# Optimization experiments

Hardware: AMD Instinct MI355X
Metric: run time of the kernel (lower is better)

The kernel has to match this reference:

```python
import jax, jax.numpy as jnp
import numpy as np

DN = ('NCHW', 'OIHW', 'NCHW')
EPS = 1e-5


def _conv(x, w, b, stride, pad):
    y = jax.lax.conv_general_dilated(x, w, (stride, stride), ((pad, pad), (pad, pad)), dimension_numbers=DN)
    return y + b[None, :, None, None]


def _convT(x, w, b):
    # PyTorch ConvTranspose2d(k=3, stride=2, padding=1, output_padding=1)
    # weight w: [in, out, kh, kw] -> flip spatial, swap in/out -> OIHW
    wt = jnp.flip(w, (2, 3)).transpose(1, 0, 2, 3)
    y = jax.lax.conv_general_dilated(x, wt, (1, 1), ((1, 2), (1, 2)), lhs_dilation=(2, 2), dimension_numbers=DN)
    return y + b[None, :, None, None]


def _inorm(x):
    # InstanceNorm2d, affine=False, biased variance (num_features arg unused since no affine)
    m = x.mean((2, 3), keepdims=True)
    v = ((x - m) ** 2).mean((2, 3), keepdims=True)
    return (x - m) / jnp.sqrt(v + EPS)


def _lrelu(x):
    return jnp.where(x >= 0, x, 0.2 * x)


def _refpad(x):
    return jnp.pad(x, ((0, 0), (0, 0), (1, 1), (1, 1)), mode='reflect')


def _backbone(image, w1, b1, w2, b2, w3, b3, wt, bt, w4, b4):
    x = _lrelu(_inorm(_conv(_refpad(image), w1, b1, 1, 0)))   # [B,32,H,W]
    x = _lrelu(_inorm(_conv(x, w2, b2, 2, 1)))                 # [B,64,H/2,W/2]
    x = _lrelu(_inorm(_conv(x, w3, b3, 2, 1)))                 # [B,128,H/4,W/4]
    x = _lrelu(_inorm(_convT(x, wt, bt)))                      # [B,256,H/2,W/2]
    x = jnp.tanh(_conv(_refpad(x), w4, b4, 1, 0))              # [B,512,H/2,W/2]
    return x


def _style_codes(x, seg):
    # nearest interpolation of seg to (h,w): src_idx = floor(dst * H / h)
    B, C, h, w = x.shape
    H, W = seg.shape[2], seg.shape[3]
    rows = (np.arange(h) * H) // h
    cols = (np.arange(w) * W) // w
    seg_ds = seg[:, :, rows][:, :, :, cols]                    # [B,L,h,w]
    m = (seg_ds != 0).astype(x.dtype)
    sums = jnp.einsum('bchw,blhw->blc', x, m)                  # segment sums
    counts = m.sum((2, 3))[..., None]                          # [B,L,1]
    return jnp.where(counts > 0, sums / jnp.maximum(counts, 1.0), 0.0)


def setup_inputs():
    key = jax.random.key(0)
    ks = jax.random.split(key, 8)
    B, H, W, L = 8, 256, 256, 19
    image = jax.random.normal(ks[0], (B, 3, H, W), jnp.float32)
    labels = jax.random.randint(ks[1], (B, H, W), 0, L)
    seg = jax.nn.one_hot(labels, L, axis=1, dtype=jnp.float32)  # one-hot semantic map
    def w(k, shape):
        return jax.random.normal(k, shape, jnp.float32) * 0.05
    return {
        'image': image, 'seg': seg,
        'w1': w(ks[2], (32, 3, 3, 3)), 'b1': jnp.zeros(32, jnp.float32),
        'w2': w(ks[3], (64, 32, 3, 3)), 'b2': jnp.zeros(64, jnp.float32),
        'w3': w(ks[4], (128, 64, 3, 3)), 'b3': jnp.zeros(128, jnp.float32),
        'wt': w(ks[5], (128, 256, 3, 3)), 'bt': jnp.zeros(256, jnp.float32),
        'w4': w(ks[6], (512, 256, 3, 3)), 'b4': jnp.zeros(512, jnp.float32),
    }


def reference(image, seg, w1, b1, w2, b2, w3, b3, wt, bt, w4, b4):
    x = _backbone(image, w1, b1, w2, b2, w3, b3, wt, bt, w4, b4)
    return _style_codes(x, seg)  # [B, label_nc, 512]
```

## Files before the change

### kernel.cpp

```cpp
#include <hip/hip_runtime.h>
#include <hip/hip_bf16.h>
#include <math.h>

typedef __attribute__((ext_vector_type(8))) short bf16x8;
typedef __attribute__((ext_vector_type(8))) unsigned short u16x8;
typedef __attribute__((ext_vector_type(4))) float f32x4;
typedef __attribute__((ext_vector_type(2))) long longx2;

#define OFF_X1   0ull
#define OFF_XQ8  0ull
#define OFF_X2   34080768ull
#define OFF_X3   51386368ull
#define OFF_Y4   60039168ull
#define OFF_WB8  127148032ull
#define OFF_WB2  129507328ull
#define OFF_WB3  129548288ull
#define OFF_WBT  129695744ull
#define OFF_ST1  130744320ull
#define OFF_ST2  130746368ull
#define OFF_ST3  130750464ull
#define OFF_ST4  130758656ull
#define OFF_SUMS 130775040ull
#define OFF_CNT  131086336ull
#define OFF_MS1  131086944ull
#define OFF_MS2  131088992ull
#define OFF_MS3  131093088ull
#define OFF_MS4  131101280ull
#define OFF_LAB  131117664ull
#define OFF_DWS  131641952ull
#define OFF_WSM  132166240ull
#define OFF_ST5  132690528ull
#define OFF_CB   132706912ull

__device__ __forceinline__ float bfu2f(unsigned short u) {
  return __builtin_bit_cast(float, ((unsigned)u) << 16);
}
__device__ __forceinline__ unsigned short f2bfu(float f) {
  __hip_bfloat16 h = __float2bfloat16(f);
  return __builtin_bit_cast(unsigned short, h);
}
__device__ __forceinline__ void gload_lds16(const void* g, void* l) {
  __builtin_amdgcn_global_load_lds(
      (const __attribute__((address_space(1))) unsigned int*)g,
      (__attribute__((address_space(3))) unsigned int*)l, 16, 0, 0);
}
template <bool HI>
__device__ __forceinline__ int cvtpk8(float a, float b, int old) {
  return __builtin_amdgcn_cvt_pk_fp8_f32(a, b, old, HI);
}
template <int SEL>
__device__ __forceinline__ float cvtf8(int v) {
  return __builtin_amdgcn_cvt_f32_fp8(v, SEL);
}

#define WAITV(N) asm volatile("s_waitcnt vmcnt(" #N ")" ::: "memory")

#define PIPE_STEP(WAITN, BUF, DOSTAGE, SNEXT)                 \
  asm volatile("s_waitcnt vmcnt(" #WAITN ")" ::: "memory");   \
  __builtin_amdgcn_s_barrier();                               \
  __builtin_amdgcn_sched_barrier(0);                          \
  mmaStep(BUF, (BUF) + 16384);                                \
  __builtin_amdgcn_sched_barrier(0);                          \
  __builtin_amdgcn_s_barrier();                               \
  if (DOSTAGE) stage(SNEXT, BUF);

__global__ __launch_bounds__(256) void padz_k(unsigned short* __restrict__ x1,
                                              unsigned short* __restrict__ x2,
                                              unsigned short* __restrict__ x3) {
  int u = blockIdx.x * 256 + threadIdx.x;
  int b = u / 10368, r = u % 10368;
  u16x8 z = {0, 0, 0, 0, 0, 0, 0, 0};
  if (r < 4128) {
    unsigned short* base = x1 + (size_t)b * 2130048;
    if (r < 2064) {
      int row = r < 1032 ? 0 : 257, pos = r < 1032 ? r : r - 1032;
      base += (row * 258 + (pos >> 2)) * 32 + (pos & 3) * 8;
    } else {
      int rc = r - 2064;
      int col = rc < 1032 ? 0 : 257, pos = rc < 1032 ? rc : rc - 1032;
      base += ((pos >> 2) * 258 + col) * 32 + (pos & 3) * 8;
    }
    *(u16x8*)base = z;
  } else if (r < 8288) {
    int s = r - 4128;
    unsigned short* base = x2 + (size_t)b * 1081600;
    if (s < 2080) {
      int row = s < 1040 ? 0 : 129, pos = s < 1040 ? s : s - 1040;
      base += (row * 130 + (pos >> 3)) * 64 + (pos & 7) * 8;
    } else {
      int sc = s - 2080;
      int col = sc < 1040 ? 0 : 129, pos = sc < 1040 ? sc : sc - 1040;
      base += ((pos >> 3) * 130 + col) * 64 + (pos & 7) * 8;
    }
    *(u16x8*)base = z;
  } else {
    int t = r - 8288;
    unsigned short* base = x3 + (size_t)b * 540800;
    if (t < 1040) {
      base += (64 * 65 + (t >> 4)) * 128 + (t & 15) * 8;
    } else {
      int pos = t - 1040;
      base += ((pos >> 4) * 65 + 64) * 128 + (pos & 15) * 8;
    }
    *(u16x8*)base = z;
  }
}

__global__ __launch_bounds__(256) void conv1_k(const float* __restrict__ img,
                                               const float* __restrict__ w1,
                                               unsigned short* __restrict__ x1) {
  __shared__ float wl[864];
  int t = threadIdx.x, y = blockIdx.x, b = blockIdx.y;
  for (int i = t; i < 864; i += 256) wl[i] = w1[(i & 31) * 27 + (i >> 5)];
  __syncthreads();
  int x = t;
  float val[27];
  for (int ic = 0; ic < 3; ++ic) {
    const float* ip = img + ((size_t)(b * 3 + ic)) * 65536;
#pragma unroll
    for (int ky = 0; ky < 3; ++ky) {
      int gy = y - 1 + ky; gy = gy < 0 ? -gy : (gy > 255 ? 510 - gy : gy);
#pragma unroll
      for (int kx = 0; kx < 3; ++kx) {
        int gx = x - 1 + kx; gx = gx < 0 ? -gx : (gx > 255 ? 510 - gx : gx);
        val[ic * 9 + ky * 3 + kx] = ip[gy * 256 + gx];
      }
    }
  }
  float a[32];
#pragma unroll
  for (int oc = 0; oc < 32; ++oc) a[oc] = 0.f;
#pragma unroll
  for (int k = 0; k < 27; ++k) {
    float vv = val[k];
#pragma unroll
    for (int oc = 0; oc < 32; ++oc) a[oc] += wl[k * 32 + oc] * vv;
  }
  unsigned short ov[32];
#pragma unroll
  for (int oc = 0; oc < 32; ++oc) ov[oc] = f2bfu(a[oc]);
  unsigned short* op = x1 + ((size_t)(b * 258 + y + 1) * 258 + (x + 1)) * 32;
#pragma unroll
  for (int i = 0; i < 4; ++i) *(u16x8*)(op + i * 8) = *(const u16x8*)(ov + i * 8);
}

template <int C>
__global__ void statsn_k(const unsigned short* __restrict__ base, int rowStride, int unitsLog,
                         int rowsPer, long bStride, float* __restrict__ stats) {
  const int CH8 = C / 8;
  __shared__ float bins[C * 2];
  int tid = threadIdx.x, slice = blockIdx.x, b = blockIdx.y;
  for (int i = tid; i < C * 2; i += 256) bins[i] = 0.f;
  __syncthreads();
  const unsigned short* bp = base + (size_t)b * bStride + (size_t)(slice * rowsPer) * rowStride;
  int total = rowsPer << unitsLog;
  float s8[8] = {0, 0, 0, 0, 0, 0, 0, 0}, q8[8] = {0, 0, 0, 0, 0, 0, 0, 0};
  for (int idx = tid; idx < total; idx += 256) {
    int rl = idx >> unitsLog, ux = idx & ((1 << unitsLog) - 1);
    u16x8 v = *(const u16x8*)(bp + (size_t)rl * rowStride + ux * 8);
#pragma unroll
    for (int e = 0; e < 8; ++e) { float f = bfu2f(v[e]); s8[e] += f; q8[e] += f * f; }
  }
#pragma unroll
  for (int e = 0; e < 8; ++e)
    for (int off = 32; off >= CH8; off >>= 1) {
      s8[e] += __shfl_xor(s8[e], off);
      q8[e] += __shfl_xor(q8[e], off);
    }
  int lane = tid & 63;
  if (lane < CH8) {
#pragma unroll
    for (int e = 0; e < 8; ++e) {
      atomicAdd(&bins[(lane * 8 + e) * 2], s8[e]);
      atomicAdd(&bins[(lane * 8 + e) * 2 + 1], q8[e]);
    }
  }
  __syncthreads();
  for (int i = tid; i < C * 2; i += 256) atomicAdd(&stats[b * C * 2 + i], bins[i]);
}

__global__ void msn_k(const float* __restrict__ st, float2* __restrict__ ms, float invN, int total) {
  int i = blockIdx.x * 256 + threadIdx.x;
  if (i < total) {
    float m = st[2 * i] * invN;
    float v = st[2 * i + 1] * invN - m * m;
    ms[i] = make_float2(m, rsqrtf(fmaxf(v, 0.f) + 1e-5f));
  }
}

template <int C>
__global__ void nln_k(unsigned short* __restrict__ base, int rowStride, int unitsPerRow,
                      long bStride, const float2* __restrict__ ms) {
  const int CH8 = C / 8;
  int row = blockIdx.x, b = blockIdx.y;
  unsigned short* rp = base + (size_t)b * bStride + (size_t)row * rowStride;
  const float2* msb = ms + b * C;
  for (int idx = threadIdx.x; idx < unitsPerRow; idx += 256) {
    u16x8 v = *(u16x8*)(rp + idx * 8);
    int ch = (idx & (CH8 - 1)) * 8;
    u16x8 o;
#pragma unroll
    for (int e = 0; e < 8; ++e) {
      float2 m = msb[ch + e];
      float f = (bfu2f(v[e]) - m.x) * m.y;
      o[e] = f2bfu(f >= 0.f ? f : 0.2f * f);
    }
    *(u16x8*)(rp + idx * 8) = o;
  }
}

__global__ __launch_bounds__(256) void nln8_k(const unsigned short* __restrict__ y4,
                                              const float2* __restrict__ ms,
                                              unsigned char* __restrict__ xq8,
                                              float* __restrict__ st5) {
  __shared__ float bs[512];
  int t = threadIdx.x, row = blockIdx.x, b = blockIdx.y;
  int cg = t & 31, pg = t >> 5;
  int wof0 = (cg >> 4) * 128 + ((((cg & 15) & 3) << 2) | ((cg & 15) >> 2)) * 8;
  const float2* msb = ms + b * 256;
  float2 m0[8];
#pragma unroll
  for (int e = 0; e < 8; ++e) m0[e] = msb[cg * 8 + e];
  const unsigned short* rp = y4 + ((size_t)b * 16384 + row * 128) * 256;
  unsigned char* op = xq8 + ((size_t)b * 16384 + (size_t)row * 128) * 256;
  float s[8] = {0, 0, 0, 0, 0, 0, 0, 0}, d[8] = {0, 0, 0, 0, 0, 0, 0, 0};
  for (int i = 0; i < 16; ++i) {
    int px = pg * 16 + i;
    u16x8 v = *(const u16x8*)(rp + (size_t)px * 256 + cg * 8);
    float f[8];
#pragma unroll
    for (int e = 0; e < 8; ++e) {
      float x = (bfu2f(v[e]) - m0[e].x) * m0[e].y;
      f[e] = x >= 0.f ? x : 0.2f * x;
    }
    int lo = cvtpk8<false>(f[0], f[1], 0); lo = cvtpk8<true>(f[2], f[3], lo);
    int hi = cvtpk8<false>(f[4], f[5], 0); hi = cvtpk8<true>(f[6], f[7], hi);
    *(long*)(op + (size_t)px * 256 + wof0) =
        ((long)(unsigned)hi << 32) | (unsigned)lo;
    float fq;
    fq = cvtf8<0>(lo); s[0] += fq; d[0] += fq - f[0];
    fq = cvtf8<1>(lo); s[1] += fq; d[1] += fq - f[1];
    fq = cvtf8<2>(lo); s[2] += fq; d[2] += fq - f[2];
    fq = cvtf8<3>(lo); s[3] += fq; d[3] += fq - f[3];
    fq = cvtf8<0>(hi); s[4] += fq; d[4] += fq - f[4];
    fq = cvtf8<1>(hi); s[5] += fq; d[5] += fq - f[5];
    fq = cvtf8<2>(hi); s[6] += fq; d[6] += fq - f[6];
    fq = cvtf8<3>(hi); s[7] += fq; d[7] += fq - f[7];
  }
  for (int i = t; i < 512; i += 256) bs[i] = 0.f;
  __syncthreads();
#pragma unroll
  for (int e = 0; e < 8; ++e) {
    atomicAdd(&bs[cg * 8 + e], s[e]);
    atomicAdd(&bs[256 + cg * 8 + e], d[e]);
  }
  __syncthreads();
  for (int i = t; i < 512; i += 256) atomicAdd(&st5[b * 512 + i], bs[i]);
}

__global__ void wrep2_k(const float* __restrict__ w2, unsigned short* __restrict__ wb2) {
  int idx = blockIdx.x * 256 + threadIdx.x;
  if (idx >= 20480) return;
  int oc = idx / 320, r = idx % 320, tap = r >> 5, ic = r & 31;
  wb2[idx] = tap < 9 ? f2bfu(w2[(oc * 32 + ic) * 9 + tap]) : (unsigned short)0;
}
__global__ void wrep3_k(const float* __restrict__ w3, unsigned short* __restrict__ wb3) {
  int idx = blockIdx.x * 256 + threadIdx.x;
  int oc = idx / 576, r = idx % 576, tap = r >> 6, ic = r & 63;
  wb3[idx] = f2bfu(w3[(oc * 64 + ic) * 9 + tap]);
}
__device__ const int c_taptab[16] = {4, -1, -1, -1, 5, 3, -1, -1, 7, -1, 1, -1, 8, 6, 2, 0};
__global__ void wrepT_k(const float* __restrict__ wt, unsigned short* __restrict__ wbt) {
  int idx = blockIdx.x * 256 + threadIdx.x;
  int n = idx >> 9, k = idx & 511;
  int cl = n >> 8, oc = n & 255, nb = k >> 7, ic = k & 127;
  int tap = c_taptab[cl * 4 + nb];
  wbt[idx] = tap < 0 ? (unsigned short)0 : f2bfu(wt[(ic * 256 + oc) * 9 + tap]);
}
__global__ __launch_bounds__(256) void dwrep_k(const float* __restrict__ w4,
                                               unsigned char* __restrict__ wb8,
                                               float* __restrict__ dws,
                                               float* __restrict__ wsum) {
  int oc = blockIdx.x, ic = threadIdx.x;
  int local = ic & 127;
  int p = (ic & 128) + ((local >> 3) & 3) * 32 + ((local >> 5) & 3) * 8 + (local & 7);
  float ds = 0.f, ws = 0.f;
  for (int kk = 0; kk < 9; ++kk) {
    float w = w4[(size_t)oc * 2304 + ic * 9 + kk];
    int pk = cvtpk8<false>(w, 0.f, 0);
    wb8[((size_t)oc * 9 + kk) * 256 + p] = (unsigned char)(pk & 0xff);
    float wq = cvtf8<0>(pk);
    ds += wq - w; ws += w;
  }
  dws[oc * 256 + ic] = ds;
  wsum[oc * 256 + ic] = ws;
}

__global__ __launch_bounds__(256) void cbias_k(const float* __restrict__ st5,
                                               const float* __restrict__ dws,
                                               const float* __restrict__ wsum,
                                               float* __restrict__ cb) {
  int oc = blockIdx.x, b = blockIdx.y, t = threadIdx.x;
  const float inv = 1.f / 16384.f;
  float muq = st5[b * 512 + t] * inv;
  float dmu = st5[b * 512 + 256 + t] * inv;
  float a = muq * dws[oc * 256 + t] + dmu * wsum[oc * 256 + t];
#pragma unroll
  for (int o = 1; o < 64; o <<= 1) a += __shfl_xor(a, o);
  __shared__ float r[4];
  if ((t & 63) == 0) r[t >> 6] = a;
  __syncthreads();
  if (t == 0) cb[b * 512 + oc] = r[0] + r[1] + r[2] + r[3];
}

__global__ __launch_bounds__(256) void conv2_k(const unsigned short* __restrict__ x1,
                                               const unsigned short* __restrict__ wb2,
                                               unsigned short* __restrict__ x2,
                                               float* __restrict__ st2) {
  __shared__ char smem[49664];
  float* bins = (float*)(smem + 49152);
  int tid = threadIdx.x, y = blockIdx.x, b = blockIdx.y;
  int lane = tid & 63, w = tid >> 6, wm = w >> 1, wn = w & 1;
  int lr = lane & 15, lg = lane >> 4;
  f32x4 acc[4][2];
#pragma unroll
  for (int i = 0; i < 4; ++i)
#pragma unroll
    for (int j = 0; j < 2; ++j) acc[i][j] = (f32x4){0.f, 0.f, 0.f, 0.f};

  int rowA[4], lcA[4], PbA[4];
#pragma unroll
  for (int i = 0; i < 4; ++i) {
    int pb = i * 256 + tid;
    PbA[i] = pb * 16; rowA[i] = pb >> 3; lcA[i] = (pb & 7) ^ (rowA[i] & 7);
  }
  int rowB[2], lcB[2], PbB[2];
#pragma unroll
  for (int i = 0; i < 2; ++i) {
    int pb = i * 256 + tid;
    PbB[i] = pb * 16; rowB[i] = pb >> 3; lcB[i] = (pb & 7) ^ (rowB[i] & 7);
  }
  const unsigned short* xb = x1 + (size_t)b * 2130048;

  auto stage = [&](int kb, char* base) {
    char* As = base;
    char* Bs = base + 16384;
#pragma unroll
    for (int i = 0; i < 4; ++i) {
      int tp = kb * 2 + (lcA[i] >> 2);
      int ky = (tp * 11) >> 5;
      int kx = tp - ky * 3;
      gload_lds16(xb + ((size_t)((2 * y + ky) * 258 + 2 * rowA[i] + kx)) * 32 + (lcA[i] & 3) * 8,
                  As + PbA[i]);
    }
#pragma unroll
    for (int i = 0; i < 2; ++i)
      gload_lds16(wb2 + rowB[i] * 320 + kb * 64 + lcB[i] * 8, Bs + PbB[i]);
  };

  stage(0, smem);
  __syncthreads();
  for (int kb = 0; kb < 5; ++kb) {
    char* base = smem + (kb & 1) * 24576;
    if (kb + 1 < 5) stage(kb + 1, smem + ((kb + 1) & 1) * 24576);
    char* As = base;
    char* Bs = base + 16384;
    bf16x8 af[4][2], bfr[2][2];
#pragma unroll
    for (int mi = 0; mi < 4; ++mi)
#pragma unroll
      for (int kh = 0; kh < 2; ++kh) {
        int row = wm * 64 + mi * 16 + lr;
        int byte = row * 128 + ((kh * 64 + lg * 16) ^ ((row & 7) << 4));
        af[mi][kh] = *(const bf16x8*)(As + byte);
      }
#pragma unroll
    for (int ni = 0; ni < 2; ++ni)
#pragma unroll
      for (int kh = 0; kh < 2; ++kh) {
        int row = wn * 32 + ni * 16 + lr;
        int byte = row * 128 + ((kh * 64 + lg * 16) ^ ((row & 7) << 4));
        bfr[ni][kh] = *(const bf16x8*)(Bs + byte);
      }
#pragma unroll
    for (int mi = 0; mi < 4; ++mi)
#pragma unroll
      for (int ni = 0; ni < 2; ++ni)
#pragma unroll
        for (int kh = 0; kh < 2; ++kh)
          acc[mi][ni] = __builtin_amdgcn_mfma_f32_16x16x32_bf16(af[mi][kh], bfr[ni][kh],
                                                                acc[mi][ni], 0, 0, 0);
    __syncthreads();
  }

  if (tid < 128) bins[tid] = 0.f;
  __syncthreads();
  unsigned short* ob = x2 + (size_t)b * 1081600;
#pragma unroll
  for (int ni = 0; ni < 2; ++ni) {
    int oc = wn * 32 + ni * 16 + lr;
    float s = 0.f, q = 0.f;
#pragma unroll
    for (int mi = 0; mi < 4; ++mi)
#pragma unroll
      for (int r = 0; r < 4; ++r) {
        int m = wm * 64 + mi * 16 + lg * 4 + r;
        float v = acc[mi][ni][r];
        ob[((y + 1) * 130 + m + 1) * 64 + oc] = f2bfu(v);
        s += v; q += v * v;
      }
    atomicAdd(&bins[oc * 2], s);
    atomicAdd(&bins[oc * 2 + 1], q);
  }
  __syncthreads();
  if (tid < 128) atomicAdd(&st2[b * 128 + tid], bins[tid]);
}

__global__ __launch_bounds__(256) void conv3_k(const unsigned short* __restrict__ x2,
                                               const unsigned short* __restrict__ wb3,
                                               unsigned short* __restrict__ x3,
                                               float* __restrict__ st3) {
  __shared__ char smem[66560];
  float* bins = (float*)(smem + 65536);
  int tid = threadIdx.x, y0 = blockIdx.x * 2, b = blockIdx.y;
  int lane = tid & 63, w = tid >> 6, wm = w >> 1, wn = w & 1;
  int lr = lane & 15, lg = lane >> 4;
  f32x4 acc[4][4];
#pragma unroll
  for (int i = 0; i < 4; ++i)
#pragma unroll
    for (int j = 0; j < 4; ++j) acc[i][j] = (f32x4){0.f, 0.f, 0.f, 0.f};

  int rowS[4], lc[4], Pb[4];
#pragma unroll
  for (int i = 0; i < 4; ++i) {
    int pb = i * 256 + tid;
    Pb[i] = pb * 16; rowS[i] = pb >> 3; lc[i] = (pb & 7) ^ (rowS[i] & 7);
  }
  const unsigned short* xb = x2 + (size_t)b * 1081600;

  auto stage = [&](int kk, char* base) {
    int ky = kk / 3, kx = kk - ky * 3;
#pragma unroll
    for (int i = 0; i < 4; ++i) {
      int m = rowS[i], di = m >> 6, xx = m & 63;
      gload_lds16(xb + ((size_t)((2 * (y0 + di) + ky) * 130 + 2 * xx + kx)) * 64 + lc[i] * 8,
                  base + Pb[i]);
    }
#pragma unroll
    for (int i = 0; i < 4; ++i)
      gload_lds16(wb3 + (rowS[i] * 9 + kk) * 64 + lc[i] * 8, base + 16384 + Pb[i]);
  };

  stage(0, smem);
  __syncthreads();
  for (int kk = 0; kk < 9; ++kk) {
    char* base = smem + (kk & 1) * 32768;
    if (kk + 1 < 9) stage(kk + 1, smem + ((kk + 1) & 1) * 32768);
    char* As = base;
    char* Bs = base + 16384;
    bf16x8 af[4][2], bfr[4][2];
#pragma unroll
    for (int mi = 0; mi < 4; ++mi)
#pragma unroll
      for (int kh = 0; kh < 2; ++kh) {
        int row = wm * 64 + mi * 16 + lr;
        int byte = row * 128 + ((kh * 64 + lg * 16) ^ ((row & 7) << 4));
        af[mi][kh] = *(const bf16x8*)(As + byte);
      }
#pragma unroll
    for (int ni = 0; ni < 4; ++ni)
#pragma unroll
      for (int kh = 0; kh < 2; ++kh) {
        int row = wn * 64 + ni * 16 + lr;
        int byte = row * 128 + ((kh * 64 + lg * 16) ^ ((row & 7) << 4));
        bfr[ni][kh] = *(const bf16x8*)(Bs + byte);
      }
#pragma unroll
    for (int mi = 0; mi < 4; ++mi)
#pragma unroll
      for (int ni = 0; ni < 4; ++ni)
#pragma unroll
        for (int kh = 0; kh < 2; ++kh)
          acc[mi][ni] = __builtin_amdgcn_mfma_f32_16x16x32_bf16(af[mi][kh], bfr[ni][kh],
                                                                acc[mi][ni], 0, 0, 0);
    __syncthreads();
  }

  if (tid < 256) bins[tid] = 0.f;
  __syncthreads();
  unsigned short* ob = x3 + (size_t)b * 540800;
#pragma unroll
  for (int ni = 0; ni < 4; ++ni) {
    int oc = wn * 64 + ni * 16 + lr;
    float s = 0.f, q = 0.f;
#pragma unroll
    for (int mi = 0; mi < 4; ++mi)
#pragma unroll
      for (int r = 0; r < 4; ++r) {
        int m = wm * 64 + mi * 16 + lg * 4 + r;
        int di = m >> 6, xx = m & 63;
        float v = acc[mi][ni][r];
        ob[((y0 + di) * 65 + xx) * 128 + oc] = f2bfu(v);
        s += v; q += v * v;
      }
    atomicAdd(&bins[oc * 2], s);
    atomicAdd(&bins[oc * 2 + 1], q);
  }
  __syncthreads();
  if (tid < 256) atomicAdd(&st3[b * 256 + tid], bins[tid]);
}

__global__ __launch_bounds__(256) void convT_k(const unsigned short* __restrict__ x3,
                                               const unsigned short* __restrict__ wbt,
                                               unsigned short* __restrict__ y4,
                                               float* __restrict__ st4) {
  __shared__ char smem[67584];
  float* bins = (float*)(smem + 65536);
  int tid = threadIdx.x, i0 = blockIdx.x * 2, nblk = blockIdx.y, b = blockIdx.z;
  int n0 = nblk * 128, cl = nblk >> 1, och0 = (nblk & 1) * 128;
  int lane = tid & 63, w = tid >> 6, wm = w >> 1, wn = w & 1;
  int lr = lane & 15, lg = lane >> 4;
  f32x4 acc[4][4];
#pragma unroll
  for (int i = 0; i < 4; ++i)
#pragma unroll
    for (int j = 0; j < 4; ++j) acc[i][j] = (f32x4){0.f, 0.f, 0.f, 0.f};

  int rowS[4], lc[4], Pb[4];
#pragma unroll
  for (int i = 0; i < 4; ++i) {
    int pb = i * 256 + tid;
    Pb[i] = pb * 16; rowS[i] = pb >> 3; lc[i] = (pb & 7) ^ (rowS[i] & 7);
  }
  int aoff[4][2], boff[4][2];
#pragma unroll
  for (int mi = 0; mi < 4; ++mi)
#pragma unroll
    for (int kh = 0; kh < 2; ++kh) {
      int row = wm * 64 + mi * 16 + lr;
      aoff[mi][kh] = row * 128 + ((kh * 64 + lg * 16) ^ ((row & 7) << 4));
      int rowb = wn * 64 + mi * 16 + lr;
      boff[mi][kh] = rowb * 128 + ((kh * 64 + lg * 16) ^ ((rowb & 7) << 4));
    }
  const unsigned short* xb = x3 + (size_t)b * 540800;

  auto stage = [&](int kb, char* base) {
    int nb = kb >> 1, chalf = (kb & 1) * 64;
#pragma unroll
    for (int i = 0; i < 4; ++i) {
      int m = rowS[i], di = m >> 6, j = m & 63;
      int pi = i0 + di + (nb >> 1), pj = j + (nb & 1);
      gload_lds16(xb + ((size_t)(pi * 65 + pj)) * 128 + chalf + lc[i] * 8, base + Pb[i]);
    }
#pragma unroll
    for (int i = 0; i < 4; ++i)
      gload_lds16(wbt + (size_t)(n0 + rowS[i]) * 512 + kb * 64 + lc[i] * 8,
                  base + 16384 + Pb[i]);
  };

  auto mmaStep = [&](char* As, char* Bs) {
    bf16x8 af[4][2], bfr[4][2];
#pragma unroll
    for (int mi = 0; mi < 4; ++mi)
#pragma unroll
      for (int kh = 0; kh < 2; ++kh) af[mi][kh] = *(const bf16x8*)(As + aoff[mi][kh]);
#pragma unroll
    for (int ni = 0; ni < 4; ++ni)
#pragma unroll
      for (int kh = 0; kh < 2; ++kh) bfr[ni][kh] = *(const bf16x8*)(Bs + boff[ni][kh]);
#pragma unroll
    for (int mi = 0; mi < 4; ++mi)
#pragma unroll
      for (int ni = 0; ni < 4; ++ni)
#pragma unroll
        for (int kh = 0; kh < 2; ++kh)
          acc[mi][ni] = __builtin_amdgcn_mfma_f32_16x16x32_bf16(af[mi][kh], bfr[ni][kh],
                                                                acc[mi][ni], 0, 0, 0);
  };

  char* B0 = smem;
  char* B1 = smem + 32768;
  stage(0, B0);
  stage(1, B1);
  for (int sp = 0; sp < 3; ++sp) {
    PIPE_STEP(8, B0, true, 2 * sp + 2);
    PIPE_STEP(8, B1, true, 2 * sp + 3);
  }
  PIPE_STEP(8, B0, false, 0);
  PIPE_STEP(0, B1, false, 0);

  if (tid < 256) bins[tid] = 0.f;
  __syncthreads();
  unsigned short* ob = y4 + (size_t)b * 4194304;
  int dy = cl >> 1, dx = cl & 1;
#pragma unroll
  for (int ni = 0; ni < 4; ++ni) {
    int loc = wn * 64 + ni * 16 + lr;
    int oc = och0 + loc;
    float s = 0.f, q = 0.f;
#pragma unroll
    for (int mi = 0; mi < 4; ++mi)
#pragma unroll
      for (int r = 0; r < 4; ++r) {
        int m = wm * 64 + mi * 16 + lg * 4 + r;
        int di = m >> 6, j = m & 63;
        int oy = 2 * (i0 + di) + dy, ox = 2 * j + dx;
        float v = acc[mi][ni][r];
        ob[(oy * 128 + ox) * 256 + oc] = f2bfu(v);
        s += v; q += v * v;
      }
    atomicAdd(&bins[loc * 2], s);
    atomicAdd(&bins[loc * 2 + 1], q);
  }
  __syncthreads();
  if (tid < 256) atomicAdd(&st4[b * 512 + och0 * 2 + tid], bins[tid]);
}

__global__ void lab_k(const float* __restrict__ seg, int* __restrict__ lab,
                      float* __restrict__ counts) {
  __shared__ int hist[19];
  int t = threadIdx.x;
  if (t < 19) hist[t] = 0;
  __syncthreads();
  int b = blockIdx.y;
  int p = blockIdx.x * 256 + t;
  int i = p >> 7, j = p & 127;
  const float* sp = seg + (size_t)b * 19 * 65536 + (2 * i) * 256 + 2 * j;
  int l = 0;
  for (int k = 0; k < 19; ++k) { if (sp[(size_t)k * 65536] != 0.f) { l = k; break; } }
  lab[b * 16384 + p] = l;
  atomicAdd(&hist[l], 1);
  __syncthreads();
  if (t < 19) atomicAdd(&counts[b * 19 + t], (float)hist[t]);
}

__global__ __launch_bounds__(256, 3) void conv4_k(
    const unsigned char* __restrict__ xq8, const unsigned char* __restrict__ wb8,
    const float* __restrict__ b4, const float* __restrict__ cb,
    const int* __restrict__ lab, float* __restrict__ sums) {
  __shared__ char smem[33280];
  char* As = smem;
  char* Bs = smem + 16384;
  int* labs = (int*)(smem + 32768);
  int tid = threadIdx.x;
  int id = blockIdx.x;
  int b = id & 7, rr = id >> 3;
  int y = rr >> 2, nblk = rr & 3;
  int n0 = nblk * 128;
  if (tid < 128) labs[tid] = lab[b * 16384 + y * 128 + tid];
  int lane = tid & 63, w = tid >> 6;
  int wm = w >> 1, wn = w & 1;
  int lr = lane & 15, lg = lane >> 4;

  f32x4 acc[4][4];
#pragma unroll
  for (int i = 0; i < 4; ++i)
#pragma unroll
    for (int j = 0; j < 4; ++j) acc[i][j] = (f32x4){0.f, 0.f, 0.f, 0.f};

  const unsigned char* xb = xq8 + (size_t)b * 4194304;

  int rs0 = tid >> 3;
  int csw = ((tid & 7) ^ (rs0 & 7)) << 4;
  int ldoff = tid * 16;

  const unsigned char* brow[4];
#pragma unroll
  for (int i = 0; i < 4; ++i)
    brow[i] = wb8 + (size_t)(n0 + rs0 + 32 * i) * 2304 + csw;

  int koff = 0;
  for (int kk = 0; kk < 9; ++kk) {
    int ky = (kk * 11) >> 5, kx = kk - ky * 3;
    int sy = y + ky - 1; sy = sy < 0 ? 1 : (sy > 127 ? 126 : sy);
    const unsigned char* arow[4];
#pragma unroll
    for (int i = 0; i < 4; ++i) {
      int sx = rs0 + 32 * i + kx - 1;
      sx = sx < 0 ? 1 : (sx > 127 ? 126 : sx);
      arow[i] = xb + ((size_t)(sy * 128 + sx)) * 256 + csw;
    }
    for (int ic0 = 0; ic0 < 256; ic0 += 128) {
      __syncthreads();
#pragma unroll
      for (int i = 0; i < 4; ++i) gload_lds16(arow[i] + ic0, As + i * 4096 + ldoff);
#pragma unroll
      for (int i = 0; i < 4; ++i) gload_lds16(brow[i] + koff, Bs + i * 4096 + ldoff);
      koff += 128;
      __syncthreads();

      longx2 bq[4][2];
#pragma unroll
      for (int ni = 0; ni < 4; ++ni) {
        int row = wn * 64 + ni * 16 + lr;
#pragma unroll
        for (int k2 = 0; k2 < 2; ++k2) {
          int byte = row * 128 + ((lg * 32 + k2 * 16) ^ ((row & 7) << 4));
          bq[ni][k2] = *(const longx2*)(Bs + byte);
        }
      }
#pragma unroll
      for (int mi = 0; mi < 4; ++mi) {
        int row = wm * 64 + mi * 16 + lr;
        longx2 aq[2];
#pragma unroll
        for (int k2 = 0; k2 < 2; ++k2) {
          int byte = row * 128 + ((lg * 32 + k2 * 16) ^ ((row & 7) << 4));
          aq[k2] = *(const longx2*)(As + byte);
        }
#pragma unroll
        for (int ni = 0; ni < 4; ++ni)
#pragma unroll
          for (int k2 = 0; k2 < 2; ++k2) {
            acc[mi][ni] = __builtin_amdgcn_mfma_f32_16x16x32_fp8_fp8(
                aq[k2][0], bq[ni][k2][0], acc[mi][ni], 0, 0, 0);
            acc[mi][ni] = __builtin_amdgcn_mfma_f32_16x16x32_fp8_fp8(
                aq[k2][1], bq[ni][k2][1], acc[mi][ni], 0, 0, 0);
          }
      }
    }
  }

  __syncthreads();
  float* bins = (float*)smem;
  for (int t2 = tid; t2 < 19 * 128; t2 += 256) bins[t2] = 0.f;
  __syncthreads();
  float bias[4];
#pragma unroll
  for (int ni = 0; ni < 4; ++ni) {
    int gc = n0 + wn * 64 + ni * 16 + lr;
    bias[ni] = b4[gc] - cb[b * 512 + gc];
  }
#pragma unroll
  for (int mi = 0; mi < 4; ++mi)
#pragma unroll
    for (int ni = 0; ni < 4; ++ni) {
      int ct = wn * 64 + ni * 16 + lr;
#pragma unroll
      for (int r = 0; r < 4; ++r) {
        int x = wm * 64 + mi * 16 + lg * 4 + r;
        float v = tanhf(acc[mi][ni][r] + bias[ni]);
        atomicAdd(&bins[labs[x] * 128 + ct], v);
      }
    }
  __syncthreads();
  for (int t2 = tid; t2 < 19 * 128; t2 += 256) {
    float v = bins[t2];
    if (v != 0.f)
      atomicAdd(&sums[((size_t)(b * 19 + (t2 >> 7))) * 512 + n0 + (t2 & 127)], v);
  }
}

__global__ void finalize_k(const float* __restrict__ sums, const float* __restrict__ counts,
                           float* __restrict__ out) {
  int idx = blockIdx.x * 256 + threadIdx.x;
  int bl = idx / 512;
  float c = counts[bl];
  out[idx] = c > 0.f ? sums[idx] / fmaxf(c, 1.f) : 0.f;
}

extern "C" void kernel_launch(void* const* d_in, const int* in_sizes, int n_in,
                              void* d_out, int out_size, void* d_ws, size_t ws_size,
                              hipStream_t stream) {
  const float* image = (const float*)d_in[0];
  const float* seg   = (const float*)d_in[1];
  const float* w1    = (const float*)d_in[2];
  const float* w2    = (const float*)d_in[4];
  const float* w3    = (const float*)d_in[6];
  const float* wt    = (const float*)d_in[8];
  const float* w4    = (const float*)d_in[10];
  const float* b4    = (const float*)d_in[11];
  float* out = (float*)d_out;
  char* ws = (char*)d_ws;

  unsigned short* x1  = (unsigned short*)(ws + OFF_X1);
  unsigned char*  xq8 = (unsigned char*)(ws + OFF_XQ8);
  unsigned short* x2  = (unsigned short*)(ws + OFF_X2);
  unsigned short* x3  = (unsigned short*)(ws + OFF_X3);
  unsigned short* y4  = (unsigned short*)(ws + OFF_Y4);
  unsigned char*  wb8 = (unsigned char*)(ws + OFF_WB8);
  unsigned short* wb2 = (unsigned short*)(ws + OFF_WB2);
  unsigned short* wb3 = (unsigned short*)(ws + OFF_WB3);
  unsigned short* wbt = (unsigned short*)(ws + OFF_WBT);
  float* st1 = (float*)(ws + OFF_ST1);
  float* st2 = (float*)(ws + OFF_ST2);
  float* st3 = (float*)(ws + OFF_ST3);
  float* st4 = (float*)(ws + OFF_ST4);
  float* sums = (float*)(ws + OFF_SUMS);
  float* counts = (float*)(ws + OFF_CNT);
  float2* ms1 = (float2*)(ws + OFF_MS1);
  float2* ms2 = (float2*)(ws + OFF_MS2);
  float2* ms3 = (float2*)(ws + OFF_MS3);
  float2* ms4 = (float2*)(ws + OFF_MS4);
  int* lab = (int*)(ws + OFF_LAB);
  float* dws  = (float*)(ws + OFF_DWS);
  float* wsum = (float*)(ws + OFF_WSM);
  float* st5  = (float*)(ws + OFF_ST5);
  float* cbv  = (float*)(ws + OFF_CB);

  padz_k<<<324, 256, 0, stream>>>(x1, x2, x3);
  hipMemsetAsync(ws + OFF_ST1, 0, 342624, stream);
  hipMemsetAsync(ws + OFF_ST5, 0, 16384, stream);

  wrep2_k<<<80, 256, 0, stream>>>(w2, wb2);
  wrep3_k<<<288, 256, 0, stream>>>(w3, wb3);
  wrepT_k<<<2048, 256, 0, stream>>>(wt, wbt);
  dwrep_k<<<512, 256, 0, stream>>>(w4, wb8, dws, wsum);
  lab_k<<<dim3(64, 8), 256, 0, stream>>>(seg, lab, counts);

  conv1_k<<<dim3(256, 8), 256, 0, stream>>>(image, w1, x1);
  statsn_k<32><<<dim3(16, 8), 256, 0, stream>>>(x1 + 259 * 32, 258 * 32, 10, 16, 2130048L, st1);
  msn_k<<<1, 256, 0, stream>>>(st1, ms1, 1.f / 65536.f, 256);
  nln_k<32><<<dim3(256, 8), 256, 0, stream>>>(x1 + 259 * 32, 258 * 32, 1024, 2130048L, ms1);

  conv2_k<<<dim3(128, 8), 256, 0, stream>>>(x1, wb2, x2, st2);
  msn_k<<<2, 256, 0, stream>>>(st2, ms2, 1.f / 16384.f, 512);
  nln_k<64><<<dim3(128, 8), 256, 0, stream>>>(x2 + 131 * 64, 130 * 64, 1024, 1081600L, ms2);

  conv3_k<<<dim3(32, 8), 256, 0, stream>>>(x2, wb3, x3, st3);
  msn_k<<<4, 256, 0, stream>>>(st3, ms3, 1.f / 4096.f, 1024);
  nln_k<128><<<dim3(64, 8), 256, 0, stream>>>(x3, 65 * 128, 1024, 540800L, ms3);

  convT_k<<<dim3(32, 8, 8), 256, 0, stream>>>(x3, wbt, y4, st4);
  msn_k<<<8, 256, 0, stream>>>(st4, ms4, 1.f / 16384.f, 2048);

  nln8_k<<<dim3(128, 8), 256, 0, stream>>>(y4, ms4, xq8, st5);
  cbias_k<<<dim3(512, 8), 256, 0, stream>>>(st5, dws, wsum, cbv);

  conv4_k<<<4096, 256, 0, stream>>>(xq8, wb8, b4, cbv, lab, sums);

  finalize_k<<<304, 256, 0, stream>>>(sums, counts, out);
}
```

Measured before the change: 733.8 us.

## Double-buffer A tiles in LDS and read B weights directly from global

The conv4 GEMM main loop now double-buffers the activation (A) tile in LDS, prefetching the next K-step while computing the current one, and uses one barrier per step instead of two. The weight (B) operand is no longer staged through LDS; each lane loads its MFMA fragments straight from global memory, relying on cache reuse across blocks. Launch bounds are raised to 4 waves-per-SIMD occupancy. This trades LDS traffic and barrier stalls for uncoalesced direct global loads of weights and tighter register budgets.

```diff
diff --git a/kernel.cpp b/kernel.cpp
--- a/kernel.cpp
+++ b/kernel.cpp
@@ -635,13 +635,11 @@
   if (t < 19) atomicAdd(&counts[b * 19 + t], (float)hist[t]);
 }
 
-__global__ __launch_bounds__(256, 3) void conv4_k(
+__global__ __launch_bounds__(256, 4) void conv4_k(
     const unsigned char* __restrict__ xq8, const unsigned char* __restrict__ wb8,
     const float* __restrict__ b4, const float* __restrict__ cb,
     const int* __restrict__ lab, float* __restrict__ sums) {
   __shared__ char smem[33280];
-  char* As = smem;
-  char* Bs = smem + 16384;
   int* labs = (int*)(smem + 32768);
   int tid = threadIdx.x;
   int id = blockIdx.x;
@@ -665,64 +663,66 @@
   int csw = ((tid & 7) ^ (rs0 & 7)) << 4;
   int ldoff = tid * 16;
 
-  const unsigned char* brow[4];
-#pragma unroll
-  for (int i = 0; i < 4; ++i)
-    brow[i] = wb8 + (size_t)(n0 + rs0 + 32 * i) * 2304 + csw;
-
-  int koff = 0;
-  for (int kk = 0; kk < 9; ++kk) {
+  const unsigned char* bb[4];
+#pragma unroll
+  for (int ni = 0; ni < 4; ++ni)
+    bb[ni] = wb8 + (size_t)(n0 + wn * 64 + ni * 16 + lr) * 2304 + lg * 32;
+
+  int aoffL[4][2];
+#pragma unroll
+  for (int mi = 0; mi < 4; ++mi)
+#pragma unroll
+    for (int k2 = 0; k2 < 2; ++k2) {
+      int row = wm * 64 + mi * 16 + lr;
+      aoffL[mi][k2] = row * 128 + ((lg * 32 + k2 * 16) ^ ((row & 7) << 4));
+    }
+
+  auto stageA = [&](int t, char* dst) {
+    int kk = t >> 1, ic0 = (t & 1) << 7;
     int ky = (kk * 11) >> 5, kx = kk - ky * 3;
     int sy = y + ky - 1; sy = sy < 0 ? 1 : (sy > 127 ? 126 : sy);
-    const unsigned char* arow[4];
 #pragma unroll
     for (int i = 0; i < 4; ++i) {
       int sx = rs0 + 32 * i + kx - 1;
       sx = sx < 0 ? 1 : (sx > 127 ? 126 : sx);
-      arow[i] = xb + ((size_t)(sy * 128 + sx)) * 256 + csw;
-    }
-    for (int ic0 = 0; ic0 < 256; ic0 += 128) {
-      __syncthreads();
-#pragma unroll
-      for (int i = 0; i < 4; ++i) gload_lds16(arow[i] + ic0, As + i * 4096 + ldoff);
-#pragma unroll
-      for (int i = 0; i < 4; ++i) gload_lds16(brow[i] + koff, Bs + i * 4096 + ldoff);
-      koff += 128;
-      __syncthreads();
-
-      longx2 bq[4][2];
-#pragma unroll
-      for (int ni = 0; ni < 4; ++ni) {
-        int row = wn * 64 + ni * 16 + lr;
+      gload_lds16(xb + ((size_t)(sy * 128 + sx)) * 256 + ic0 + csw, dst + i * 4096 + ldoff);
+    }
+  };
+
+  char* buf0 = smem;
+  char* buf1 = smem + 16384;
+  stageA(0, buf0);
+  __syncthreads();
+  for (int s = 0; s < 18; ++s) {
+    char* cur = (s & 1) ? buf1 : buf0;
+    char* nxt = (s & 1) ? buf0 : buf1;
+    if (s + 1 < 18) stageA(s + 1, nxt);
+
+    longx2 bq[4][2];
+#pragma unroll
+    for (int ni = 0; ni < 4; ++ni)
+#pragma unroll
+      for (int k2 = 0; k2 < 2; ++k2)
+        bq[ni][k2] = *(const longx2*)(bb[ni] + s * 128 + k2 * 16);
+
+#pragma unroll
+    for (int mi = 0; mi < 4; ++mi) {
+      longx2 aq[2];
+#pragma unroll
+      for (int k2 = 0; k2 < 2; ++k2) aq[k2] = *(const longx2*)(cur + aoffL[mi][k2]);
+#pragma unroll
+      for (int ni = 0; ni < 4; ++ni)
 #pragma unroll
         for (int k2 = 0; k2 < 2; ++k2) {
-          int byte = row * 128 + ((lg * 32 + k2 * 16) ^ ((row & 7) << 4));
-          bq[ni][k2] = *(const longx2*)(Bs + byte);
+          acc[mi][ni] = __builtin_amdgcn_mfma_f32_16x16x32_fp8_fp8(
+              aq[k2][0], bq[ni][k2][0], acc[mi][ni], 0, 0, 0);
+          acc[mi][ni] = __builtin_amdgcn_mfma_f32_16x16x32_fp8_fp8(
+              aq[k2][1], bq[ni][k2][1], acc[mi][ni], 0, 0, 0);
         }
-      }
-#pragma unroll
-      for (int mi = 0; mi < 4; ++mi) {
-        int row = wm * 64 + mi * 16 + lr;
-        longx2 aq[2];
-#pragma unroll
-        for (int k2 = 0; k2 < 2; ++k2) {
-          int byte = row * 128 + ((lg * 32 + k2 * 16) ^ ((row & 7) << 4));
-          aq[k2] = *(const longx2*)(As + byte);
-        }
-#pragma unroll
-        for (int ni = 0; ni < 4; ++ni)
-#pragma unroll
-          for (int k2 = 0; k2 < 2; ++k2) {
-            acc[mi][ni] = __builtin_amdgcn_mfma_f32_16x16x32_fp8_fp8(
-                aq[k2][0], bq[ni][k2][0], acc[mi][ni], 0, 0, 0);
-            acc[mi][ni] = __builtin_amdgcn_mfma_f32_16x16x32_fp8_fp8(
-                aq[k2][1], bq[ni][k2][1], acc[mi][ni], 0, 0, 0);
-          }
-      }
-    }
-  }
-
-  __syncthreads();
+    }
+    __syncthreads();
+  }
+
   float* bins = (float*)smem;
   for (int t2 = tid; t2 < 19 * 128; t2 += 256) bins[t2] = 0.f;
   __syncthreads();
```

After: 886.6 us. +20.8%, slower.
